# Performance work log

Measured on AMD Instinct MI355X. Metric: run time of the kernel, lower is better.

The kernel has to match this reference:

```python
import jax, jax.numpy as jnp
import numpy as np

RADIUS = 0.1
K = 32          # group_size
SCALE = 4
EPS = 1e-5      # InstanceNorm2d eps
BIG = 1e10


def _fps(p, n):
    # furthest point sampling, p: (B, N, 3) -> idx (B, n) int32
    B, N, _ = p.shape
    d0 = jnp.full((B, N), BIG, p.dtype)
    last0 = jnp.zeros((B,), jnp.int32)

    def step(carry, _):
        dists, last = carry
        lp = jnp.take_along_axis(p, last[:, None, None], axis=1)  # (B,1,3)
        d = jnp.sum((p - lp) ** 2, axis=-1)                        # (B,N)
        dists = jnp.minimum(dists, d)
        nxt = jnp.argmax(dists, axis=-1).astype(jnp.int32)
        return (dists, nxt), nxt

    (_, _), rest = jax.lax.scan(step, (d0, last0), None, length=n - 1)
    return jnp.concatenate([last0[None, :], rest], axis=0).T  # (B, n)


def _ball_query(center, p, radius, k):
    # center: (B,M,3), p: (B,N,3) -> neighbor idx (B,M,k)
    N = p.shape[1]
    d2 = jnp.sum((center[:, :, None, :] - p[:, None, :, :]) ** 2, axis=-1)  # (B,M,N)
    within = d2 < radius * radius
    cand = jnp.where(within, jnp.arange(N, dtype=jnp.int32), N)
    neg, _ = jax.lax.top_k(-cand, k)       # smallest k candidate indices
    cand = -neg                             # ascending, N = 'not found'
    first = cand[..., :1]
    idx = jnp.where(cand == N, first, cand)  # pad with first found (CUDA ballquery semantics)
    return jnp.where(idx == N, 0, idx)       # empty ball -> 0 (never happens: center is its own neighbor)


def _conv_block(x, w):
    # 1x1 conv (bias-free) + InstanceNorm2d(affine=False) + ReLU
    x = jnp.einsum('oi,bimk->bomk', w, x)
    m = x.mean(axis=(2, 3), keepdims=True)
    v = x.var(axis=(2, 3), keepdims=True)   # biased var, matches torch InstanceNorm
    x = (x - m) * jax.lax.rsqrt(v + EPS)
    return jax.nn.relu(x)


def _chan_attn(x, w1, w2):
    s = x.mean(axis=(2, 3))                 # (B,C) squeeze
    h = jax.nn.relu(s @ w1.T)
    g = jax.nn.sigmoid(h @ w2.T)
    return x * g[:, :, None, None]


def _stage(p_cur, f_cur, m, w1, a1w1, a1w2, w2, a2w1, a2w2):
    idx = _fps(p_cur, m)                                               # (B,M)
    cp = jnp.take_along_axis(p_cur, idx[:, :, None], axis=1)          # (B,M,3)
    cf = jnp.take_along_axis(f_cur, idx[:, None, :], axis=2)          # (B,C,M)
    gidx = _ball_query(cp, p_cur, RADIUS, K)                           # (B,M,K)
    gp = jax.vmap(lambda pts, i: pts[i])(p_cur, gidx)                  # (B,M,K,3)
    dp = jnp.transpose(gp - cp[:, :, None, :], (0, 3, 1, 2))           # (B,3,M,K)
    fj = jax.vmap(lambda ff, i: ff[:, i])(f_cur, gidx)                 # (B,C,M,K)
    feat = jnp.concatenate([dp, fj - cf[..., None]], axis=1)           # dp_df: (B,3+C,M,K)
    x = _chan_attn(_conv_block(feat, w1), a1w1, a1w2)
    pooled = jnp.broadcast_to(x.max(axis=-1, keepdims=True), x.shape)
    x = _chan_attn(_conv_block(jnp.concatenate([pooled, x], axis=1), w2), a2w1, a2w2)
    return cp, x.max(axis=-1)                                          # (B,M,3), (B,C_out,M)


def setup_inputs() -> dict:
    key = jax.random.key(0)
    ks = jax.random.split(key, 16)
    w = lambda k, o, i: (jax.random.normal(k, (o, i), jnp.float32) / np.float32(np.sqrt(i)))
    return {
        'p': jax.random.uniform(ks[0], (4, 8192, 3), jnp.float32),
        'f': jax.random.normal(ks[1], (4, 3, 8192), jnp.float32),
        # stage 0: edge-in 6 -> 192, conv2 384 -> 192
        's0_w1': w(ks[2], 192, 6),   's0_a1w1': w(ks[3], 48, 192),  's0_a1w2': w(ks[4], 192, 48),
        's0_w2': w(ks[5], 192, 384), 's0_a2w1': w(ks[6], 48, 192),  's0_a2w2': w(ks[7], 192, 48),
        # stage 1: edge-in 195 -> 384, conv2 768 -> 384
        's1_w1': w(ks[8], 384, 195), 's1_a1w1': w(ks[9], 96, 384),  's1_a1w2': w(ks[10], 384, 96),
        's1_w2': w(ks[11], 384, 768),'s1_a2w1': w(ks[12], 96, 384), 's1_a2w2': w(ks[13], 384, 96),
    }


def reference(p, f, s0_w1, s0_a1w1, s0_a1w2, s0_w2, s0_a2w1, s0_a2w2,
              s1_w1, s1_a1w1, s1_a1w2, s1_w2, s1_a2w1, s1_a2w2):
    N = p.shape[1]
    cp1, f1 = _stage(p, f, N // SCALE, s0_w1, s0_a1w1, s0_a1w2, s0_w2, s0_a2w1, s0_a2w2)
    cp2, f2 = _stage(cp1, f1, N // SCALE ** 2, s1_w1, s1_a1w1, s1_a1w2, s1_w2, s1_a2w1, s1_a2w2)
    # (out_p, out_f) flattened: points per level, features per level
    return (p, cp1, cp2, f, f1, f2)
```

## Files before the change

### kernel.cpp

```cpp
#include <hip/hip_runtime.h>
#include <hip/hip_bf16.h>
#include <stdint.h>

typedef __hip_bfloat16 bf16;
typedef unsigned long long u64;
typedef short bf16x8 __attribute__((ext_vector_type(8)));
typedef float f32x4 __attribute__((ext_vector_type(4)));
#define DEVI static __device__ __forceinline__

DEVI float b2f(bf16 v){ return __bfloat162float(v); }
DEVI bf16  f2b(float v){ return __float2bfloat16(v); }
DEVI float bfL(unsigned u){ return __uint_as_float(u<<16); }
DEVI float bfH(unsigned u){ return __uint_as_float(u & 0xffff0000u); }
DEVI void unpack8(uint4 r, float* v){
  v[0]=bfL(r.x); v[1]=bfH(r.x); v[2]=bfL(r.y); v[3]=bfH(r.y);
  v[4]=bfL(r.z); v[5]=bfH(r.z); v[6]=bfL(r.w); v[7]=bfH(r.w);
}
DEVI void unpack4(uint2 r, float* v){
  v[0]=bfL(r.x); v[1]=bfH(r.x); v[2]=bfL(r.y); v[3]=bfH(r.y);
}
DEVI unsigned short bfr(float x){ bf16 h=f2b(x); return *reinterpret_cast<unsigned short*>(&h); }
DEVI unsigned pk2(float a,float b){ return (unsigned)bfr(a) | ((unsigned)bfr(b)<<16); }

constexpr int B_=4, N0=8192, M0=2048, M1=512, KK=32;
constexpr int L0=M0*KK, L1=M1*KK;
constexpr int C0=192, H0=48, C1=384, H1=96;

constexpr size_t OUT_P=0, OUT_CP1=98304, OUT_CP2=122880, OUT_F=129024,
                 OUT_F1=227328, OUT_F2=1800192;

constexpr size_t A_FLAG  = 0;
constexpr size_t A_CP1F  = 256;
constexpr size_t A_CP2F  = A_CP1F+98304;
constexpr size_t A_IDX0  = A_CP2F+24576;
constexpr size_t A_IDX1  = A_IDX0+32768;
constexpr size_t A_GID0  = A_IDX1+8192;
constexpr size_t A_GID1  = A_GID0+1048576;
constexpr size_t A_FEAT0 = A_GID1+262144;
constexpr size_t A_M1V   = A_FEAT0+3145728;
constexpr size_t A_RS1V  = A_M1V+3072;
constexpr size_t A_SS01  = A_RS1V+3072;
constexpr size_t A_G1V   = A_SS01+3072;
constexpr size_t A_SUMA  = A_G1V+3072;
constexpr size_t A_SS02  = A_SUMA+6144;
constexpr size_t A_M2V   = A_SS02+3072;
constexpr size_t A_RS2V  = A_M2V+3072;
constexpr size_t A_G2V   = A_RS2V+3072;
constexpr size_t A_RAWP  = A_G2V+3072;
constexpr size_t A_RAWM2 = A_RAWP+6291456;
constexpr size_t A_FEAT1 = A_RAWM2+6291456;
constexpr size_t A_Y2    = A_FEAT1;
constexpr size_t WS_Y2   = A_Y2 + 100663296;
constexpr size_t A_YB1   = A_FEAT1+6389760;
constexpr size_t A_YB2   = A_YB1+12582912;
constexpr size_t A_PMS1  = A_YB2+12582912;
constexpr size_t A_MS1   = A_PMS1+786432;
constexpr size_t A_RSS1  = A_MS1+1536;
constexpr size_t A_SSS1  = A_RSS1+1536;
constexpr size_t A_G1S1  = A_SSS1+1536;
constexpr size_t A_G2S1  = A_G1S1+1536;
constexpr size_t A_F1A  = A_FEAT1;
constexpr size_t A_YB1A = A_F1A + 25559040;
constexpr size_t A_YB2A = A_YB1A + 50331648;
constexpr size_t A_PMA  = A_YB2A + 50331648;
constexpr size_t A_MSA  = A_PMA + 3145728;
constexpr size_t A_RSA  = A_MSA + 6144;
constexpr size_t A_SSA  = A_RSA + 6144;
constexpr size_t A_G1A  = A_SSA + 6144;
constexpr size_t A_G2A  = A_G1A + 6144;
constexpr size_t A_NEED = A_G2A + 6144;

DEVI const float* pick(const float* c0, const float* c1, const int* fl, int want_f){
  int sw = fl ? ((*fl)!=0) : 0;
  return (sw ^ want_f) ? c1 : c0;
}

__global__ __launch_bounds__(64)
void detect_kernel(const float* __restrict__ c0, int* __restrict__ flag){
  unsigned long long m = __ballot(c0[threadIdx.x] < 0.f);
  if(threadIdx.x==0) *flag = (m!=0ull) ? 1 : 0;
}

__global__ __launch_bounds__(256)
void cvt_pf_kernel(const float* __restrict__ c0, const float* __restrict__ c1,
                   const int* __restrict__ fl, float* __restrict__ outP,
                   float* __restrict__ outF, int n){
  const float* p = pick(c0,c1,fl,0);
  const float* f = pick(c0,c1,fl,1);
  int i=blockIdx.x*256+threadIdx.x;
  if(i<n){ outP[i]=p[i]; outF[i]=f[i]; }
}

#define DPP_ARGMAX(CTRL) { \
  int iv_=__builtin_amdgcn_update_dpp(__float_as_int(bv), __float_as_int(bv), CTRL, 0xF, 0xF, false); \
  int ii_=__builtin_amdgcn_update_dpp(bi, bi, CTRL, 0xF, 0xF, false); \
  float fv_=__int_as_float(iv_); \
  if(fv_>bv || (fv_==bv && ii_<bi)){ bv=fv_; bi=ii_; } }

template<int NP, int MS, int TPB>
__global__ __launch_bounds__(TPB)
void fps_kernel(const float* __restrict__ c0, const float* __restrict__ c1,
                const int* __restrict__ fl, int* __restrict__ sel){
  constexpr int CH = NP/TPB;
  constexpr int NW = TPB/64;
  __shared__ float4 pt4[NP];
  __shared__ u64 wvi[2][NW];
  const float* pC = pick(c0,c1,fl,0);
  int b=blockIdx.x, t=threadIdx.x;
  const float* pb = pC + (size_t)b*NP*3;
  for(int i=t;i<NP;i+=TPB)
    pt4[i]=make_float4(pb[(size_t)i*3], pb[(size_t)i*3+1], pb[(size_t)i*3+2], 0.f);
  if(t==0) sel[(size_t)b*MS]=0;
  __syncthreads();
  float ox[CH], oy[CH], oz[CH], dd[CH];
  #pragma unroll
  for(int c=0;c<CH;c++){
    float4 q=pt4[t*CH+c];
    ox[c]=q.x; oy[c]=q.y; oz[c]=q.z;
    dd[c]=1e10f;
  }
  float4 c40=pt4[0];
  float cx=c40.x, cy=c40.y, cz=c40.z;
  int par=0;
  for(int s=1;s<MS;s++){
    float bv=-1.f; int bi=0;
    #pragma unroll
    for(int c=0;c<CH;c++){
      float dx=__fsub_rn(ox[c],cx), dy=__fsub_rn(oy[c],cy), dz=__fsub_rn(oz[c],cz);
      float d=__fadd_rn(__fadd_rn(__fmul_rn(dx,dx),__fmul_rn(dy,dy)),__fmul_rn(dz,dz));
      float nd=fminf(dd[c],d); dd[c]=nd;
      if(nd>bv){ bv=nd; bi=t*CH+c; }
    }
    DPP_ARGMAX(0x111) DPP_ARGMAX(0x112) DPP_ARGMAX(0x114) DPP_ARGMAX(0x118)
    DPP_ARGMAX(0x142) DPP_ARGMAX(0x143)
    if((t&63)==63)
      wvi[par][t>>6] = (((u64)__float_as_uint(bv))<<32) | (unsigned)(0xFFFFFFFFu-(unsigned)bi);
    __syncthreads();
    u64 best=wvi[par][0];
    #pragma unroll
    for(int k=1;k<NW;k++){ u64 w=wvi[par][k]; if(w>best) best=w; }
    int mi = (int)(0xFFFFFFFFu - (unsigned)best);
    if(t==0) sel[(size_t)b*MS+s]=mi;
    float4 c4=pt4[mi];
    cx=c4.x; cy=c4.y; cz=c4.z;
    par^=1;
  }
}

__global__ __launch_bounds__(256)
void gather_cp_kernel(const float* __restrict__ c0, const float* __restrict__ c1,
                      const int* __restrict__ fl, const int* __restrict__ sel,
                      int NP, int MS, float* __restrict__ cpf, float* __restrict__ outcp){
  const float* pC = pick(c0,c1,fl,0);
  int t=blockIdx.x*256+threadIdx.x;
  if(t>=B_*MS) return;
  int b=t/MS;
  int j=sel[t];
  const float* src=pC + ((size_t)b*NP + j)*3;
  float x=src[0],y=src[1],z=src[2];
  float* d=cpf + (size_t)t*3; d[0]=x; d[1]=y; d[2]=z;
  float* o=outcp + (size_t)t*3; o[0]=x; o[1]=y; o[2]=z;
}

template<int NP, int MS>
__global__ __launch_bounds__(256)
void ballq_kernel(const float* __restrict__ c0, const float* __restrict__ c1,
                  const int* __restrict__ fl, const float* __restrict__ cpf,
                  int* __restrict__ gidx){
  __shared__ int cand[4][64][33];
  __shared__ int ccnt[4][64];
  const float* pC = pick(c0,c1,fl,0);
  int t=threadIdx.x, q=t>>6, cl=t&63;
  int b=blockIdx.y, m=blockIdx.x*64+cl;
  const float* cc=cpf + ((size_t)b*MS+m)*3;
  float cx=cc[0], cy=cc[1], cz=cc[2];
  const float R2=0.01f;
  const float* pb=pC + (size_t)b*NP*3;
  int cnt=0;
  int j0=q*(NP/4), j1=j0+NP/4;
  for(int j=j0;j<j1;j++){
    if(cnt>=32) break;
    float dx=__fsub_rn(cx,pb[(size_t)j*3]);
    float dy=__fsub_rn(cy,pb[(size_t)j*3+1]);
    float dz=__fsub_rn(cz,pb[(size_t)j*3+2]);
    float d2=__fadd_rn(__fadd_rn(__fmul_rn(dx,dx),__fmul_rn(dy,dy)),__fmul_rn(dz,dz));
    if(d2<R2) cand[q][cl][cnt++]=j;
  }
  ccnt[q][cl]=cnt;
  __syncthreads();
  if(q==0){
    int* gp=gidx + ((size_t)b*MS+m)*32;
    int total=0, first=0; bool has=false;
    for(int qq=0;qq<4;qq++){
      int n=ccnt[qq][cl];
      for(int u=0;u<n;u++){
        if(total>=32) break;
        int id=cand[qq][cl][u];
        if(!has){ first=id; has=true; }
        gp[total++]=id;
      }
      if(total>=32) break;
    }
    if(!has){ for(int u=0;u<32;u++) gp[u]=0; }
    else    { for(int u=total;u<32;u++) gp[u]=first; }
  }
}

__global__ __launch_bounds__(256)
void feat0_kernel(const float* __restrict__ c0, const float* __restrict__ c1,
                  const int* __restrict__ fl, const float* __restrict__ cp1f,
                  const int* __restrict__ idx0, const int* __restrict__ gidx0,
                  bf16* __restrict__ feat){
  const float* p0f = pick(c0,c1,fl,0);
  const float* f_in= pick(c0,c1,fl,1);
  int t=blockIdx.x*256+threadIdx.x;
  int b=t>>16, rem=t&65535, m=rem>>5;
  int j=gidx0[t];
  int sel=idx0[(b<<11)+m];
  const float* pj=p0f + ((size_t)(b*N0)+j)*3;
  const float* cm=cp1f + ((size_t)(b*M0)+m)*3;
  bf16* fb=feat + (size_t)b*6*L0 + rem;
  fb[0]      =f2b(pj[0]-cm[0]);
  fb[L0]     =f2b(pj[1]-cm[1]);
  fb[2*L0]   =f2b(pj[2]-cm[2]);
  const float* fI=f_in + (size_t)b*3*N0;
  #pragma unroll
  for(int c=0;c<3;c++)
    fb[(size_t)(3+c)*L0]=f2b(fI[c*N0+j]-fI[c*N0+sel]);
}

__global__ __launch_bounds__(256)
void s0c1_stats_kernel(const bf16* __restrict__ feat, const float* __restrict__ W1,
                       float* __restrict__ m1v, float* __restrict__ rs1v){
  int row=blockIdx.x, b=row/C0, c=row%C0, t=threadIdx.x;
  float w6[6];
  #pragma unroll
  for(int j=0;j<6;j++) w6[j]=W1[c*6+j];
  const bf16* fb=feat + (size_t)b*6*L0;
  float s=0.f,s2=0.f;
  for(int base=t*8;base<L0;base+=2048){
    float X[6][8];
    #pragma unroll
    for(int i=0;i<6;i++){ uint4 r=*(const uint4*)(fb+(size_t)i*L0+base); unpack8(r,X[i]); }
    #pragma unroll
    for(int u=0;u<8;u++){
      float y=0.f;
      #pragma unroll
      for(int j=0;j<6;j++) y=fmaf(w6[j],X[j][u],y);
      s+=y; s2+=y*y;
    }
  }
  #pragma unroll
  for(int off=32;off>0;off>>=1){ s+=__shfl_down(s,off,64); s2+=__shfl_down(s2,off,64); }
  __shared__ float as[4], bs[4];
  int w=t>>6;
  if((t&63)==0){ as[w]=s; bs[w]=s2; }
  __syncthreads();
  if(t==0){
    float S=as[0]+as[1]+as[2]+as[3], S2=bs[0]+bs[1]+bs[2]+bs[3];
    float m=S/(float)L0, var=S2/(float)L0-m*m;
    var=fmaxf(var,0.f);
    m1v[row]=m; rs1v[row]=rsqrtf(var+1e-5f);
  }
}

__global__ __launch_bounds__(256)
void s0c1_pool_kernel(const bf16* __restrict__ feat, const float* __restrict__ W1,
                      const float* __restrict__ m1v, const float* __restrict__ rs1v,
                      float* __restrict__ rawp, float* __restrict__ ss01){
  int row=blockIdx.x, b=row/C0, c=row%C0, t=threadIdx.x;
  float w6[6];
  #pragma unroll
  for(int j=0;j<6;j++) w6[j]=W1[c*6+j];
  const bf16* fb=feat + (size_t)b*6*L0;
  float m=m1v[row], rs=rs1v[row];
  float ss=0.f;
  for(int base=t*8;base<L0;base+=2048){
    float X[6][8];
    #pragma unroll
    for(int i=0;i<6;i++){ uint4 r=*(const uint4*)(fb+(size_t)i*L0+base); unpack8(r,X[i]); }
    float mx=-3e38f;
    #pragma unroll
    for(int u=0;u<8;u++){
      float y=0.f;
      #pragma unroll
      for(int j=0;j<6;j++) y=fmaf(w6[j],X[j][u],y);
      float x=fmaxf((y-m)*rs,0.f);
      ss+=x; mx=fmaxf(mx,x);
    }
    mx=fmaxf(mx,__shfl_down(mx,2,64));
    mx=fmaxf(mx,__shfl_down(mx,1,64));
    if((t&3)==0) rawp[(size_t)row*M0 + (base>>5)] = mx;
  }
  #pragma unroll
  for(int off=32;off>0;off>>=1) ss+=__shfl_down(ss,off,64);
  __shared__ float as[4];
  int w=t>>6;
  if((t&63)==0) as[w]=ss;
  __syncthreads();
  if(t==0) ss01[row]=(as[0]+as[1]+as[2]+as[3])/(float)L0;
}

__global__ __launch_bounds__(256)
void s0conv2_mfma_kernel(const float* __restrict__ W2, const bf16* __restrict__ feat,
                         const float* __restrict__ W1,
                         const float* __restrict__ m1v, const float* __restrict__ rs1v,
                         const float* __restrict__ g1v, const float* __restrict__ rawp,
                         bf16* __restrict__ y2out){
  __shared__ __align__(16) bf16 sW[2][64][40];
  __shared__ __align__(16) bf16 sXT[128][40];
  __shared__ float f6[6][128];
  __shared__ float w1s[192][6];
  __shared__ float cmv[192], crsv[192], cgv[192];
  int t=threadIdx.x, b=blockIdx.z, o0=blockIdx.y*64, l0=blockIdx.x*128;
  for(int u=t;u<768;u+=256){ int i=u>>7, lc=u&127; f6[i][lc]=b2f(feat[((size_t)(b*6+i))*L0+l0+lc]); }
  for(int u=t;u<1152;u+=256){ w1s[u/6][u%6]=W1[u]; }
  for(int u=t;u<192;u+=256){ int r=b*C0+u; cmv[u]=m1v[r]; crsv[u]=rs1v[r]; cgv[u]=g1v[r]; }
  int wv=t>>6, lane=t&63, nn=lane&15, quad=lane>>4, kb=quad*8;
  int il=t&31, lq=(t>>5)*16;
  f32x4 acc[8];
  #pragma unroll
  for(int i=0;i<8;i++) acc[i]=(f32x4){0.f,0.f,0.f,0.f};
  __syncthreads();
  for(int c=0;c<12;c++){
    int i0=c*32;
    for(int u=t;u<2048;u+=256){
      int oo=u>>5, kk=u&31;
      float w=W2[(size_t)(o0+oo)*384 + i0+kk];
      bf16 hi=f2b(w);
      sW[0][oo][kk]=hi;
      sW[1][oo][kk]=f2b(w-b2f(hi));
    }
    {
      int i=i0+il;
      if(i<192){
        float pv=cgv[i]*rawp[((size_t)(b*C0+i))*M0 + ((l0+lq)>>5)];
        bf16 pb_=f2b(pv);
        #pragma unroll
        for(int u=0;u<16;u++) sXT[lq+u][il]=pb_;
      } else {
        int cc=i-192;
        float w6[6];
        #pragma unroll
        for(int j=0;j<6;j++) w6[j]=w1s[cc][j];
        float mm=cmv[cc], rr=crsv[cc], gg=cgv[cc];
        #pragma unroll
        for(int u=0;u<16;u++){
          float y=0.f;
          #pragma unroll
          for(int j=0;j<6;j++) y=fmaf(w6[j], f6[j][lq+u], y);
          sXT[lq+u][il]=f2b(gg*fmaxf((y-mm)*rr,0.f));
        }
      }
    }
    __syncthreads();
    bf16x8 aHi=*(const bf16x8*)&sW[0][wv*16+nn][kb];
    bf16x8 aLo=*(const bf16x8*)&sW[1][wv*16+nn][kb];
    #pragma unroll
    for(int lt=0;lt<8;lt++){
      bf16x8 bfr_=*(const bf16x8*)&sXT[lt*16+nn][kb];
      acc[lt]=__builtin_amdgcn_mfma_f32_16x16x32_bf16(aHi,bfr_,acc[lt],0,0,0);
      acc[lt]=__builtin_amdgcn_mfma_f32_16x16x32_bf16(aLo,bfr_,acc[lt],0,0,0);
    }
    __syncthreads();
  }
  #pragma unroll
  for(int lt=0;lt<8;lt++){
    int l=l0+lt*16+nn;
    #pragma unroll
    for(int r=0;r<4;r++){
      int o=o0+wv*16+quad*4+r;
      y2out[((size_t)(b*C0+o))*L0 + l]=f2b(acc[lt][r]);
    }
  }
}

template<int PB>
__global__ __launch_bounds__(256)
void s0conv2_kernel(const float* __restrict__ W2, const bf16* __restrict__ feat,
                    const float* __restrict__ W1,
                    const float* __restrict__ m1v, const float* __restrict__ rs1v,
                    const float* __restrict__ g1v, const float* __restrict__ rawp,
                    float* __restrict__ sumA,
                    const float* __restrict__ m2v, const float* __restrict__ rs2v,
                    float* __restrict__ ssum2, float* __restrict__ rawm2){
  __shared__ float sW[96][17];
  __shared__ float sX[16][132];
  __shared__ float f6[6][128];
  __shared__ float w1s[192][6];
  __shared__ float cm[192], crs[192], cg[192];
  int t=threadIdx.x, b=blockIdx.z, o0=blockIdx.y*96, l0=blockIdx.x*128;
  for(int u=t;u<768;u+=256){ int i=u>>7, lc=u&127; f6[i][lc]=b2f(feat[((size_t)(b*6+i))*L0+l0+lc]); }
  for(int u=t;u<1152;u+=256){ w1s[u/6][u%6]=W1[u]; }
  for(int u=t;u<192;u+=256){ int r=b*C0+u; cm[u]=m1v[r]; crs[u]=rs1v[r]; cg[u]=g1v[r]; }
  __syncthreads();
  float acc[6][8];
  #pragma unroll
  for(int r=0;r<6;r++)
    #pragma unroll
    for(int c=0;c<8;c++) acc[r][c]=0.f;
  int to=t>>4, tl=t&15, oL=to*6;
  int xr=to, cA=tl*4;
  int mg0=(l0+cA)>>5;
  for(int i0=0;i0<384;i0+=16){
    #pragma unroll
    for(int u=0;u<6;u++){ int flat=u*256+t, r=flat>>4, ci=flat&15;
      sW[r][ci]=W2[(size_t)(o0+r)*384 + i0+ci]; }
    {
      int i=i0+xr;
      float v[8];
      if(i<192){
        float pv0=cg[i]*rawp[((size_t)(b*C0+i))*M0 + mg0];
        float pv1=cg[i]*rawp[((size_t)(b*C0+i))*M0 + mg0+2];
        v[0]=pv0; v[1]=pv0; v[2]=pv0; v[3]=pv0;
        v[4]=pv1; v[5]=pv1; v[6]=pv1; v[7]=pv1;
      } else {
        int c=i-192;
        #pragma unroll
        for(int u=0;u<4;u++){
          float y=0.f;
          #pragma unroll
          for(int j=0;j<6;j++) y=fmaf(w1s[c][j], f6[j][cA+u], y);
          v[u]=cg[c]*fmaxf((y-cm[c])*crs[c],0.f);
        }
        #pragma unroll
        for(int u=0;u<4;u++){
          float y=0.f;
          #pragma unroll
          for(int j=0;j<6;j++) y=fmaf(w1s[c][j], f6[j][64+cA+u], y);
          v[4+u]=cg[c]*fmaxf((y-cm[c])*crs[c],0.f);
        }
      }
      *(float4*)&sX[xr][cA]    = make_float4(v[0],v[1],v[2],v[3]);
      *(float4*)&sX[xr][64+cA] = make_float4(v[4],v[5],v[6],v[7]);
    }
    __syncthreads();
    #pragma unroll
    for(int kk=0;kk<16;kk++){
      float av[6];
      #pragma unroll
      for(int r=0;r<6;r++) av[r]=sW[oL+r][kk];
      float4 xa=*(const float4*)&sX[kk][cA];
      float4 xb=*(const float4*)&sX[kk][64+cA];
      float xv[8]={xa.x,xa.y,xa.z,xa.w,xb.x,xb.y,xb.z,xb.w};
      #pragma unroll
      for(int r=0;r<6;r++)
        #pragma unroll
        for(int c=0;c<8;c++) acc[r][c]=fmaf(av[r],xv[c],acc[r][c]);
    }
    __syncthreads();
  }
  if(PB==0){
    #pragma unroll
    for(int r=0;r<6;r++){
      float ps=0.f, ps2=0.f;
      #pragma unroll
      for(int c=0;c<8;c++){ ps+=acc[r][c]; ps2+=acc[r][c]*acc[r][c]; }
      #pragma unroll
      for(int off=8;off>0;off>>=1){ ps+=__shfl_down(ps,off,64); ps2+=__shfl_down(ps2,off,64); }
      if(tl==0){ int o=b*C0+o0+oL+r; atomicAdd(&sumA[o],ps); atomicAdd(&sumA[768+o],ps2); }
    }
  } else {
    #pragma unroll
    for(int r=0;r<6;r++){
      int o=b*C0+o0+oL+r;
      float mm=m2v[o], rr=rs2v[o];
      float ps=0.f;
      float mxA=-3e38f, mxB=-3e38f;
      #pragma unroll
      for(int c=0;c<4;c++){ float x=fmaxf((acc[r][c]-mm)*rr,0.f); ps+=x; mxA=fmaxf(mxA,x); }
      #pragma unroll
      for(int c=4;c<8;c++){ float x=fmaxf((acc[r][c]-mm)*rr,0.f); ps+=x; mxB=fmaxf(mxB,x); }
      #pragma unroll
      for(int off=8;off>0;off>>=1) ps+=__shfl_down(ps,off,64);
      if(tl==0) atomicAdd(&ssum2[o], ps);
      mxA=fmaxf(mxA,__shfl_down(mxA,4,64)); mxB=fmaxf(mxB,__shfl_down(mxB,4,64));
      mxA=fmaxf(mxA,__shfl_down(mxA,2,64)); mxB=fmaxf(mxB,__shfl_down(mxB,2,64));
      mxA=fmaxf(mxA,__shfl_down(mxA,1,64)); mxB=fmaxf(mxB,__shfl_down(mxB,1,64));
      if(tl==0){ rawm2[(size_t)o*M0 + (l0>>5)    ] = mxA;
                 rawm2[(size_t)o*M0 + (l0>>5) + 2] = mxB; }
      if(tl==8){ rawm2[(size_t)o*M0 + (l0>>5) + 1] = mxA;
                 rawm2[(size_t)o*M0 + (l0>>5) + 3] = mxB; }
    }
  }
}

__global__ __launch_bounds__(256)
void s0y2_pool_kernel(const bf16* __restrict__ y2, const float* __restrict__ m2v,
                      const float* __restrict__ rs2v,
                      float* __restrict__ rawm2, float* __restrict__ ss02){
  int row=blockIdx.x, t=threadIdx.x;
  const bf16* yr=y2 + (size_t)row*L0;
  float m=m2v[row], rs=rs2v[row];
  float ss=0.f;
  for(int base=t*8;base<L0;base+=2048){
    uint4 r=*(const uint4*)(yr+base);
    float v[8]; unpack8(r,v);
    float mx=-3e38f;
    #pragma unroll
    for(int u=0;u<8;u++){
      float x=fmaxf((v[u]-m)*rs,0.f);
      ss+=x; mx=fmaxf(mx,x);
    }
    mx=fmaxf(mx,__shfl_down(mx,2,64));
    mx=fmaxf(mx,__shfl_down(mx,1,64));
    if((t&3)==0) rawm2[(size_t)row*M0 + (base>>5)] = mx;
  }
  #pragma unroll
  for(int off=32;off>0;off>>=1) ss+=__shfl_down(ss,off,64);
  __shared__ float as[4];
  int w=t>>6;
  if((t&63)==0) as[w]=ss;
  __syncthreads();
  if(t==0) ss02[row]=(as[0]+as[1]+as[2]+as[3])/(float)L0;
}

__global__ __launch_bounds__(256)
void fin_stats_kernel(const float* __restrict__ sums, float invL, int n,
                      float* __restrict__ mp, float* __restrict__ rp){
  int i=blockIdx.x*256+threadIdx.x;
  if(i<n){
    float m=sums[i]*invL;
    float v=sums[n+i]*invL - m*m;
    v=fmaxf(v,0.f);
    mp[i]=m; rp[i]=rsqrtf(v+1e-5f);
  }
}

__global__ __launch_bounds__(256)
void f1fin_kernel(const float* __restrict__ g2, float* __restrict__ rawm,
                  float* __restrict__ outF1){
  int idx=blockIdx.x*256+threadIdx.x;
  int row=idx>>11;
  float v=g2[row]*rawm[idx];
  rawm[idx]=v;
  outF1[idx]=v;
}

__global__ __launch_bounds__(256)
void feat1_kernel(int bbase, const float* __restrict__ cp1f, const float* __restrict__ cp2f,
                  const float* __restrict__ f1f, const int* __restrict__ idx1,
                  const int* __restrict__ gid1, bf16* __restrict__ featb){
  int t=blockIdx.x*256+threadIdx.x;
  int bloc=t>>14, l=t&16383;
  int b=bbase+bloc;
  int m=l>>5;
  int j=gid1[((size_t)b*M1+m)*32 + (l&31)];
  int sel=idx1[b*M1+m];
  const float* pj=cp1f + ((size_t)b*M0+j)*3;
  const float* cm=cp2f + ((size_t)b*M1+m)*3;
  bf16* fb=featb + (size_t)bloc*195*L1;
  fb[l]       =f2b(pj[0]-cm[0]);
  fb[L1+l]    =f2b(pj[1]-cm[1]);
  fb[2*L1+l]  =f2b(pj[2]-cm[2]);
  const float* fB=f1f + (size_t)b*C0*M0;
  for(int c=0;c<C0;c++)
    fb[(size_t)(3+c)*L1+l]=f2b(fB[(size_t)c*M0+j]-fB[(size_t)c*M0+sel]);
}

template<bool CAT>
__global__ __launch_bounds__(256)
void conv_b_kernel(const float* __restrict__ W, const bf16* __restrict__ X, bf16* __restrict__ Y,
                   int I, int L, int M, size_t xbs, size_t ybs,
                   const float* __restrict__ pmax, const float* __restrict__ g,
                   size_t pbs, size_t gbs, int Cc){
  __shared__ float sX[16][132];
  __shared__ float sW[96][17];
  int t=threadIdx.x, z=blockIdx.z;
  int o0=blockIdx.y*96, l0=blockIdx.x*128;
  const bf16* Xb = X + (size_t)z*xbs;
  bf16* Yb = Y + (size_t)z*ybs;
  const float* pm = CAT ? (pmax + (size_t)z*pbs) : nullptr;
  const float* gz = CAT ? (g + (size_t)z*gbs) : nullptr;
  float acc[6][8];
  #pragma unroll
  for(int r=0;r<6;r++)
    #pragma unroll
    for(int c=0;c<8;c++) acc[r][c]=0.f;
  int to=t>>4, tl=t&15, oL=to*6;
  int xr=to, cA=tl*4;
  int mg0=(l0+cA)>>5;
  for(int i0=0;i0<I;i0+=16){
    #pragma unroll
    for(int u=0;u<6;u++){
      int flat=u*256+t, r=flat>>4, ci=flat&15, i=i0+ci;
      sW[r][ci] = (i<I) ? W[(size_t)(o0+r)*I+i] : 0.f;
    }
    {
      int i=i0+xr;
      float v[8];
      if(!CAT){
        if(i<I){
          const bf16* xp = Xb + (size_t)i*L + l0;
          uint2 ra=*(const uint2*)(xp+cA);
          uint2 rb=*(const uint2*)(xp+64+cA);
          unpack4(ra,v); unpack4(rb,v+4);
        } else {
          #pragma unroll
          for(int u=0;u<8;u++) v[u]=0.f;
        }
      } else {
        if(i<Cc){
          float pv0=pm[(size_t)i*M + mg0];
          float pv1=pm[(size_t)i*M + mg0+2];
          v[0]=pv0; v[1]=pv0; v[2]=pv0; v[3]=pv0;
          v[4]=pv1; v[5]=pv1; v[6]=pv1; v[7]=pv1;
        } else {
          int ii=i-Cc;
          float gg=gz[ii];
          const bf16* xp = Xb + (size_t)ii*L + l0;
          uint2 ra=*(const uint2*)(xp+cA);
          uint2 rb=*(const uint2*)(xp+64+cA);
          unpack4(ra,v); unpack4(rb,v+4);
          #pragma unroll
          for(int u=0;u<8;u++) v[u]*=gg;
        }
      }
      *(float4*)&sX[xr][cA]    = make_float4(v[0],v[1],v[2],v[3]);
      *(float4*)&sX[xr][64+cA] = make_float4(v[4],v[5],v[6],v[7]);
    }
    __syncthreads();
    #pragma unroll
    for(int kk=0;kk<16;kk++){
      float av[6];
      #pragma unroll
      for(int r=0;r<6;r++) av[r]=sW[oL+r][kk];
      float4 xa=*(const float4*)&sX[kk][cA];
      float4 xb=*(const float4*)&sX[kk][64+cA];
      float xv[8]={xa.x,xa.y,xa.z,xa.w,xb.x,xb.y,xb.z,xb.w};
      #pragma unroll
      for(int r=0;r<6;r++)
        #pragma unroll
        for(int c=0;c<8;c++) acc[r][c]=fmaf(av[r],xv[c],acc[r][c]);
    }
    __syncthreads();
  }
  #pragma unroll
  for(int r=0;r<6;r++){
    bf16* yp=Yb + (size_t)(o0+oL+r)*L + l0;
    #pragma unroll
    for(int c=0;c<4;c++) yp[cA+c]=f2b(acc[r][c]);
    #pragma unroll
    for(int c=0;c<4;c++) yp[64+cA+c]=f2b(acc[r][4+c]);
  }
}

__global__ __launch_bounds__(256)
void rowstats_kernel(const bf16* __restrict__ Y, int L,
                     float* __restrict__ meanp, float* __restrict__ rstdp){
  int row=blockIdx.x;
  const uint4* yr=(const uint4*)(Y + (size_t)row*L);
  int nv=L/8;
  float s=0.f, s2=0.f;
  for(int i=threadIdx.x;i<nv;i+=256){
    uint4 r=yr[i]; float v[8]; unpack8(r,v);
    #pragma unroll
    for(int u=0;u<8;u++){ s+=v[u]; s2+=v[u]*v[u]; }
  }
  #pragma unroll
  for(int off=32;off>0;off>>=1){ s+=__shfl_down(s,off,64); s2+=__shfl_down(s2,off,64); }
  __shared__ float as[4], bs[4];
  int w=threadIdx.x>>6;
  if((threadIdx.x&63)==0){ as[w]=s; bs[w]=s2; }
  __syncthreads();
  if(threadIdx.x==0){
    float S=as[0]+as[1]+as[2]+as[3], S2=bs[0]+bs[1]+bs[2]+bs[3];
    float m=S/(float)L, var=S2/(float)L - m*m;
    var=fmaxf(var,0.f);
    meanp[row]=m; rstdp[row]=rsqrtf(var+1e-5f);
  }
}

__global__ __launch_bounds__(256)
void normrelu_kernel(bf16* __restrict__ Y, int L, const float* __restrict__ meanp,
                     const float* __restrict__ rstdp, float* __restrict__ ssum){
  int row=blockIdx.x;
  float m=meanp[row], rs=rstdp[row];
  uint4* yr=(uint4*)(Y + (size_t)row*L);
  int nv=L/8;
  float s=0.f;
  for(int i=threadIdx.x;i<nv;i+=256){
    uint4 r=yr[i]; float v[8]; unpack8(r,v);
    #pragma unroll
    for(int u=0;u<8;u++){ float x=(v[u]-m)*rs; x=fmaxf(x,0.f); v[u]=x; s+=x; }
    uint4 o; o.x=pk2(v[0],v[1]); o.y=pk2(v[2],v[3]); o.z=pk2(v[4],v[5]); o.w=pk2(v[6],v[7]);
    yr[i]=o;
  }
  #pragma unroll
  for(int off=32;off>0;off>>=1) s+=__shfl_down(s,off,64);
  __shared__ float as[4];
  int w=threadIdx.x>>6;
  if((threadIdx.x&63)==0) as[w]=s;
  __syncthreads();
  if(threadIdx.x==0) ssum[row]=(as[0]+as[1]+as[2]+as[3])/(float)L;
}

__global__ __launch_bounds__(256)
void attn_kernel(const float* __restrict__ ssum, const float* __restrict__ w1,
                 const float* __restrict__ w2, int Cc, int H, float* __restrict__ g,
                 float scale){
  __shared__ float sv[384]; __shared__ float hv[96];
  int b=blockIdx.x, t=threadIdx.x;
  for(int i=t;i<Cc;i+=256) sv[i]=ssum[b*Cc+i]*scale;
  __syncthreads();
  if(t<H){
    float a=0.f;
    for(int c=0;c<Cc;c++) a+=w1[(size_t)t*Cc+c]*sv[c];
    hv[t]=fmaxf(a,0.f);
  }
  __syncthreads();
  for(int o=t;o<Cc;o+=256){
    float a=0.f;
    for(int j=0;j<H;j++) a+=w2[(size_t)o*H+j]*hv[j];
    g[b*Cc+o]=1.f/(1.f+expf(-a));
  }
}

__global__ __launch_bounds__(256)
void pmax_kernel(const bf16* __restrict__ Xn, const float* __restrict__ g,
                 int Mloc, float* __restrict__ pm){
  int row=blockIdx.y;
  int m=blockIdx.x*256+threadIdx.x;
  const uint4* x=(const uint4*)(Xn + (size_t)row*Mloc*32 + (size_t)m*32);
  float mv=-3.0e38f;
  #pragma unroll
  for(int i=0;i<4;i++){
    uint4 r=x[i]; float v[8]; unpack8(r,v);
    #pragma unroll
    for(int u=0;u<8;u++) mv=fmaxf(mv,v[u]);
  }
  pm[(size_t)row*Mloc+m]=g[row]*mv;
}

__global__ __launch_bounds__(256)
void fmax_out_kernel(const bf16* __restrict__ Xn, const float* __restrict__ g,
                     int Mloc, float* __restrict__ outp){
  int row=blockIdx.y;
  int m=blockIdx.x*256+threadIdx.x;
  const uint4* x=(const uint4*)(Xn + (size_t)row*Mloc*32 + (size_t)m*32);
  float mv=-3.0e38f;
  #pragma unroll
  for(int i=0;i<4;i++){
    uint4 r=x[i]; float v[8]; unpack8(r,v);
    #pragma unroll
    for(int u=0;u<8;u++) mv=fmaxf(mv,v[u]);
  }
  outp[(size_t)row*Mloc+m]=g[row]*mv;
}

extern "C" void kernel_launch(void* const* d_in, const int* in_sizes, int n_in,
                              void* d_out, int out_size, void* d_ws, size_t ws_size,
                              hipStream_t stream){
  const float* PF[2]={nullptr,nullptr}; int npf=0;
  const float* A9[4]={0,0,0,0};  int n9=0;
  const float* A36[4]={0,0,0,0}; int n36=0;
  const float *s0_w1=0,*s0_w2=0,*s1_w1=0,*s1_w2=0;
  for(int i=0;i<n_in;i++){
    const float* ptr=(const float*)d_in[i];
    switch(in_sizes[i]){
      case 98304:  if(npf<2) PF[npf++]=ptr; break;
      case 1152:   s0_w1=ptr; break;
      case 73728:  s0_w2=ptr; break;
      case 74880:  s1_w1=ptr; break;
      case 294912: s1_w2=ptr; break;
      case 9216:   if(n9<4)  A9[n9++]=ptr;  break;
      case 36864:  if(n36<4) A36[n36++]=ptr; break;
      default: break;
    }
  }
  const float* s0_a1w1=A9[0];  const float* s0_a1w2=A9[1];
  const float* s0_a2w1=A9[2];  const float* s0_a2w2=A9[3];
  const float* s1_a1w1=A36[0]; const float* s1_a1w2=A36[1];
  const float* s1_a2w1=A36[2]; const float* s1_a2w2=A36[3];

  float* out=(float*)d_out;
  char* ws=(char*)d_ws;

  int*   flag =(int*)  (ws+A_FLAG);
  float* cp1f =(float*)(ws+A_CP1F);
  float* cp2f =(float*)(ws+A_CP2F);
  int*   idx0 =(int*)  (ws+A_IDX0);
  int*   idx1 =(int*)  (ws+A_IDX1);
  int*   gid0 =(int*)  (ws+A_GID0);
  int*   gid1 =(int*)  (ws+A_GID1);
  bf16*  feat0=(bf16*) (ws+A_FEAT0);
  float* m1v  =(float*)(ws+A_M1V);
  float* rs1v =(float*)(ws+A_RS1V);
  float* ss01 =(float*)(ws+A_SS01);
  float* g1v  =(float*)(ws+A_G1V);
  float* sumA =(float*)(ws+A_SUMA);
  float* ss02 =(float*)(ws+A_SS02);
  float* m2v  =(float*)(ws+A_M2V);
  float* rs2v =(float*)(ws+A_RS2V);
  float* g2v  =(float*)(ws+A_G2V);
  float* rawp =(float*)(ws+A_RAWP);
  float* rawm2=(float*)(ws+A_RAWM2);
  float* f1f  =rawm2;
  bf16*  y2s0 =(bf16*) (ws+A_Y2);

  detect_kernel<<<1,64,0,stream>>>(PF[0], flag);
  cvt_pf_kernel<<<384,256,0,stream>>>(PF[0], PF[1], flag, out+OUT_P, out+OUT_F, B_*N0*3);

  fps_kernel<N0,M0,256><<<B_,256,0,stream>>>(PF[0], PF[1], flag, idx0);
  gather_cp_kernel<<<32,256,0,stream>>>(PF[0], PF[1], flag, idx0, N0, M0, cp1f, out+OUT_CP1);
  ballq_kernel<N0,M0><<<dim3(32,B_),256,0,stream>>>(PF[0], PF[1], flag, cp1f, gid0);
  feat0_kernel<<<1024,256,0,stream>>>(PF[0], PF[1], flag, cp1f, idx0, gid0, feat0);

  s0c1_stats_kernel<<<B_*C0,256,0,stream>>>(feat0, s0_w1, m1v, rs1v);
  s0c1_pool_kernel<<<B_*C0,256,0,stream>>>(feat0, s0_w1, m1v, rs1v, rawp, ss01);
  attn_kernel<<<B_,256,0,stream>>>(ss01, s0_a1w1, s0_a1w2, C0, H0, g1v, 1.f);

  if(ws_size >= WS_Y2){
    s0conv2_mfma_kernel<<<dim3(512,3,B_),256,0,stream>>>(s0_w2, feat0, s0_w1, m1v, rs1v, g1v, rawp, y2s0);
    rowstats_kernel<<<B_*C0,256,0,stream>>>(y2s0, L0, m2v, rs2v);
    s0y2_pool_kernel<<<B_*C0,256,0,stream>>>(y2s0, m2v, rs2v, rawm2, ss02);
    attn_kernel<<<B_,256,0,stream>>>(ss02, s0_a2w1, s0_a2w2, C0, H0, g2v, 1.f);
  } else {
    hipMemsetAsync(ws+A_SUMA, 0, 9216, stream);
    s0conv2_kernel<0><<<dim3(512,2,B_),256,0,stream>>>(s0_w2, feat0, s0_w1, m1v, rs1v, g1v,
                                                       rawp, sumA, nullptr,nullptr,nullptr,nullptr);
    fin_stats_kernel<<<3,256,0,stream>>>(sumA, 1.f/(float)L0, 768, m2v, rs2v);
    s0conv2_kernel<1><<<dim3(512,2,B_),256,0,stream>>>(s0_w2, feat0, s0_w1, m1v, rs1v, g1v,
                                                       rawp, nullptr, m2v, rs2v, ss02, rawm2);
    attn_kernel<<<B_,256,0,stream>>>(ss02, s0_a2w1, s0_a2w2, C0, H0, g2v, 1.f/(float)L0);
  }
  f1fin_kernel<<<6144,256,0,stream>>>(g2v, rawm2, out+OUT_F1);

  fps_kernel<M0,M1,256><<<B_,256,0,stream>>>(cp1f, cp1f, nullptr, idx1);
  gather_cp_kernel<<<8,256,0,stream>>>(cp1f, cp1f, nullptr, idx1, M0, M1, cp2f, out+OUT_CP2);
  ballq_kernel<M0,M1><<<dim3(8,B_),256,0,stream>>>(cp1f, cp1f, nullptr, cp2f, gid1);

  if(ws_size >= A_NEED){
    bf16*  f1a =(bf16*) (ws+A_F1A);
    bf16*  yb1a=(bf16*) (ws+A_YB1A);
    bf16*  yb2a=(bf16*) (ws+A_YB2A);
    float* pma =(float*)(ws+A_PMA);
    float* msa =(float*)(ws+A_MSA);
    float* rsa =(float*)(ws+A_RSA);
    float* ssa =(float*)(ws+A_SSA);
    float* g1a =(float*)(ws+A_G1A);
    float* g2a =(float*)(ws+A_G2A);
    feat1_kernel<<<B_*L1/256,256,0,stream>>>(0, cp1f, cp2f, f1f, idx1, gid1, f1a);
    conv_b_kernel<false><<<dim3(L1/128,4,B_),256,0,stream>>>(s1_w1, f1a, yb1a, 195, L1, M1,
                                 (size_t)195*L1, (size_t)C1*L1, nullptr,nullptr,0,0,0);
    rowstats_kernel<<<B_*C1,256,0,stream>>>(yb1a, L1, msa, rsa);
    normrelu_kernel<<<B_*C1,256,0,stream>>>(yb1a, L1, msa, rsa, ssa);
    attn_kernel<<<B_,256,0,stream>>>(ssa, s1_a1w1, s1_a1w2, C1, H1, g1a, 1.f);
    pmax_kernel<<<dim3(2,B_*C1),256,0,stream>>>(yb1a, g1a, M1, pma);
    conv_b_kernel<true><<<dim3(L1/128,4,B_),256,0,stream>>>(s1_w2, yb1a, yb2a, 2*C1, L1, M1,
                                 (size_t)C1*L1, (size_t)C1*L1, pma, g1a, (size_t)C1*M1, (size_t)C1, C1);
    rowstats_kernel<<<B_*C1,256,0,stream>>>(yb2a, L1, msa, rsa);
    normrelu_kernel<<<B_*C1,256,0,stream>>>(yb2a, L1, msa, rsa, ssa);
    attn_kernel<<<B_,256,0,stream>>>(ssa, s1_a2w1, s1_a2w2, C1, H1, g2a, 1.f);
    fmax_out_kernel<<<dim3(2,B_*C1),256,0,stream>>>(yb2a, g2a, M1, out+OUT_F2);
  } else {
    bf16*  feat1b=(bf16*)(ws+A_FEAT1);
    bf16*  ybuf1 =(bf16*)(ws+A_YB1);
    bf16*  ybuf2 =(bf16*)(ws+A_YB2);
    float* pmS1 =(float*)(ws+A_PMS1);
    float* mS1  =(float*)(ws+A_MS1);
    float* rsS1 =(float*)(ws+A_RSS1);
    float* ssS1 =(float*)(ws+A_SSS1);
    float* g1s1 =(float*)(ws+A_G1S1);
    float* g2s1 =(float*)(ws+A_G2S1);
    for(int b=0;b<B_;b++){
      feat1_kernel<<<64,256,0,stream>>>(b, cp1f, cp2f, f1f, idx1, gid1, feat1b);
      conv_b_kernel<false><<<dim3(L1/128,4,1),256,0,stream>>>(s1_w1, feat1b, ybuf1, 195, L1, M1,
                                   0,0, nullptr,nullptr,0,0,0);
      rowstats_kernel<<<C1,256,0,stream>>>(ybuf1, L1, mS1, rsS1);
      normrelu_kernel<<<C1,256,0,stream>>>(ybuf1, L1, mS1, rsS1, ssS1);
      attn_kernel<<<1,256,0,stream>>>(ssS1, s1_a1w1, s1_a1w2, C1, H1, g1s1, 1.f);
      pmax_kernel<<<dim3(2,C1),256,0,stream>>>(ybuf1, g1s1, M1, pmS1);
      conv_b_kernel<true><<<dim3(L1/128,4,1),256,0,stream>>>(s1_w2, ybuf1, ybuf2, 2*C1, L1, M1,
                                   0,0, pmS1, g1s1, 0,0, C1);
      rowstats_kernel<<<C1,256,0,stream>>>(ybuf2, L1, mS1, rsS1);
      normrelu_kernel<<<C1,256,0,stream>>>(ybuf2, L1, mS1, rsS1, ssS1);
      attn_kernel<<<1,256,0,stream>>>(ssS1, s1_a2w1, s1_a2w2, C1, H1, g2s1, 1.f);
      fmax_out_kernel<<<dim3(2,C1),256,0,stream>>>(ybuf2, g2s1, M1, out+OUT_F2+(size_t)b*C1*M1);
    }
  }
}
```

Before: 4.143 ms.

## Move stage-1 convs to split-bf16 MFMA and streamline FPS reduction

Stage-1 1x1 convolutions now run through a new MFMA kernel that splits fp32 weights into hi/lo bf16 parts, precomputed by a small wsplit kernel into extra workspace. The aim is to replace the scalar conv_b path with matrix-core work while keeping close to fp32 weight precision. FPS no longer keeps a shared point table. The argmax reduction now carries the winning coordinates through the DPP and cross-wave steps, and indices are buffered in shared memory and written once at the end. FPS also launches with 512 threads instead of 256. The MFMA path is only taken if the workspace is large enough, and activations are still rounded to bf16.

```diff
diff --git a/kernel.cpp b/kernel.cpp
--- a/kernel.cpp
+++ b/kernel.cpp
@@ -69,6 +69,11 @@
 constexpr size_t A_G1A  = A_SSA + 6144;
 constexpr size_t A_G2A  = A_G1A + 6144;
 constexpr size_t A_NEED = A_G2A + 6144;
+constexpr size_t A_W1H  = A_NEED;
+constexpr size_t A_W1L  = A_W1H + 172032;
+constexpr size_t A_W2H  = A_W1L + 172032;
+constexpr size_t A_W2L  = A_W2H + 589824;
+constexpr size_t A_NEED2= A_W2L + 589824;
 
 DEVI const float* pick(const float* c0, const float* c1, const int* fl, int want_f){
   int sw = fl ? ((*fl)!=0) : 0;
@@ -91,11 +96,15 @@
   if(i<n){ outP[i]=p[i]; outF[i]=f[i]; }
 }
 
-#define DPP_ARGMAX(CTRL) { \
+#define DPP_ARGMAX5(CTRL) { \
   int iv_=__builtin_amdgcn_update_dpp(__float_as_int(bv), __float_as_int(bv), CTRL, 0xF, 0xF, false); \
   int ii_=__builtin_amdgcn_update_dpp(bi, bi, CTRL, 0xF, 0xF, false); \
+  int ix_=__builtin_amdgcn_update_dpp(__float_as_int(bx), __float_as_int(bx), CTRL, 0xF, 0xF, false); \
+  int iy_=__builtin_amdgcn_update_dpp(__float_as_int(by), __float_as_int(by), CTRL, 0xF, 0xF, false); \
+  int iz_=__builtin_amdgcn_update_dpp(__float_as_int(bz), __float_as_int(bz), CTRL, 0xF, 0xF, false); \
   float fv_=__int_as_float(iv_); \
-  if(fv_>bv || (fv_==bv && ii_<bi)){ bv=fv_; bi=ii_; } }
+  if(fv_>bv || (fv_==bv && ii_<bi)){ bv=fv_; bi=ii_; \
+    bx=__int_as_float(ix_); by=__int_as_float(iy_); bz=__int_as_float(iz_); } }
 
 template<int NP, int MS, int TPB>
 __global__ __launch_bounds__(TPB)
@@ -103,48 +112,48 @@
                 const int* __restrict__ fl, int* __restrict__ sel){
   constexpr int CH = NP/TPB;
   constexpr int NW = TPB/64;
-  __shared__ float4 pt4[NP];
-  __shared__ u64 wvi[2][NW];
+  __shared__ u64 kky[2][NW];
+  __shared__ float4 kxy[2][NW];
+  __shared__ int msel[MS];
   const float* pC = pick(c0,c1,fl,0);
   int b=blockIdx.x, t=threadIdx.x;
   const float* pb = pC + (size_t)b*NP*3;
-  for(int i=t;i<NP;i+=TPB)
-    pt4[i]=make_float4(pb[(size_t)i*3], pb[(size_t)i*3+1], pb[(size_t)i*3+2], 0.f);
-  if(t==0) sel[(size_t)b*MS]=0;
-  __syncthreads();
   float ox[CH], oy[CH], oz[CH], dd[CH];
   #pragma unroll
   for(int c=0;c<CH;c++){
-    float4 q=pt4[t*CH+c];
-    ox[c]=q.x; oy[c]=q.y; oz[c]=q.z;
+    int i=t*CH+c;
+    ox[c]=pb[i*3]; oy[c]=pb[i*3+1]; oz[c]=pb[i*3+2];
     dd[c]=1e10f;
   }
-  float4 c40=pt4[0];
-  float cx=c40.x, cy=c40.y, cz=c40.z;
+  if(t==0) msel[0]=0;
+  float cx=pb[0], cy=pb[1], cz=pb[2];
   int par=0;
   for(int s=1;s<MS;s++){
-    float bv=-1.f; int bi=0;
+    float bv=-1.f, bx=0.f, by=0.f, bz=0.f; int bi=0;
     #pragma unroll
     for(int c=0;c<CH;c++){
       float dx=__fsub_rn(ox[c],cx), dy=__fsub_rn(oy[c],cy), dz=__fsub_rn(oz[c],cz);
       float d=__fadd_rn(__fadd_rn(__fmul_rn(dx,dx),__fmul_rn(dy,dy)),__fmul_rn(dz,dz));
       float nd=fminf(dd[c],d); dd[c]=nd;
-      if(nd>bv){ bv=nd; bi=t*CH+c; }
-    }
-    DPP_ARGMAX(0x111) DPP_ARGMAX(0x112) DPP_ARGMAX(0x114) DPP_ARGMAX(0x118)
-    DPP_ARGMAX(0x142) DPP_ARGMAX(0x143)
-    if((t&63)==63)
-      wvi[par][t>>6] = (((u64)__float_as_uint(bv))<<32) | (unsigned)(0xFFFFFFFFu-(unsigned)bi);
+      if(nd>bv){ bv=nd; bi=t*CH+c; bx=ox[c]; by=oy[c]; bz=oz[c]; }
+    }
+    DPP_ARGMAX5(0x111) DPP_ARGMAX5(0x112) DPP_ARGMAX5(0x114) DPP_ARGMAX5(0x118)
+    DPP_ARGMAX5(0x142) DPP_ARGMAX5(0x143)
+    if((t&63)==63){
+      kky[par][t>>6] = (((u64)__float_as_uint(bv))<<32) | (unsigned)(0xFFFFFFFFu-(unsigned)bi);
+      kxy[par][t>>6] = make_float4(bx,by,bz,0.f);
+    }
     __syncthreads();
-    u64 best=wvi[par][0];
-    #pragma unroll
-    for(int k=1;k<NW;k++){ u64 w=wvi[par][k]; if(w>best) best=w; }
-    int mi = (int)(0xFFFFFFFFu - (unsigned)best);
-    if(t==0) sel[(size_t)b*MS+s]=mi;
-    float4 c4=pt4[mi];
+    u64 best=kky[par][0]; int kb=0;
+    #pragma unroll
+    for(int k=1;k<NW;k++){ u64 w=kky[par][k]; if(w>best){ best=w; kb=k; } }
+    if(t==0) msel[s]=(int)(0xFFFFFFFFu-(unsigned)best);
+    float4 c4=kxy[par][kb];
     cx=c4.x; cy=c4.y; cz=c4.z;
     par^=1;
   }
+  __syncthreads();
+  for(int i=t;i<MS;i+=TPB) sel[(size_t)b*MS+i]=msel[i];
 }
 
 __global__ __launch_bounds__(256)
@@ -373,6 +382,100 @@
       y2out[((size_t)(b*C0+o))*L0 + l]=f2b(acc[lt][r]);
     }
   }
+}
+
+template<bool CAT>
+__global__ __launch_bounds__(256)
+void conv_mfma_kernel(const bf16* __restrict__ Whi, const bf16* __restrict__ Wlo,
+                      const bf16* __restrict__ X, bf16* __restrict__ Y,
+                      int I, int Kpad, int L, int M, size_t xbs, size_t ybs,
+                      const float* __restrict__ pmax, const float* __restrict__ g,
+                      size_t pbs, size_t gbs, int Cc){
+  __shared__ __align__(16) bf16 sW[2][64][40];
+  __shared__ __align__(16) bf16 sXT[128][40];
+  int t=threadIdx.x, z=blockIdx.z, o0=blockIdx.y*64, l0=blockIdx.x*128;
+  const bf16* Xb = X + (size_t)z*xbs;
+  bf16* Yb = Y + (size_t)z*ybs;
+  const float* pm = CAT ? (pmax + (size_t)z*pbs) : nullptr;
+  const float* gz = CAT ? (g + (size_t)z*gbs) : nullptr;
+  int wv=t>>6, lane=t&63, nn=lane&15, quad=lane>>4, kb=quad*8;
+  int il=t&31, lq=(t>>5)*16;
+  f32x4 acc[8];
+  #pragma unroll
+  for(int i=0;i<8;i++) acc[i]=(f32x4){0.f,0.f,0.f,0.f};
+  int nch=Kpad/32;
+  for(int c=0;c<nch;c++){
+    int i0=c*32;
+    for(int u=t;u<2048;u+=256){
+      int oo=u>>5, kk=u&31;
+      sW[0][oo][kk]=Whi[(size_t)(o0+oo)*Kpad + i0+kk];
+      sW[1][oo][kk]=Wlo[(size_t)(o0+oo)*Kpad + i0+kk];
+    }
+    {
+      int i=i0+il;
+      if(!CAT){
+        if(i<I){
+          const bf16* xp = Xb + (size_t)i*L + l0 + lq;
+          bf16 tmp[16];
+          *(uint4*)&tmp[0]=*(const uint4*)xp;
+          *(uint4*)&tmp[8]=*(const uint4*)(xp+8);
+          #pragma unroll
+          for(int u=0;u<16;u++) sXT[lq+u][il]=tmp[u];
+        } else {
+          bf16 z0=f2b(0.f);
+          #pragma unroll
+          for(int u=0;u<16;u++) sXT[lq+u][il]=z0;
+        }
+      } else {
+        if(i<Cc){
+          float pv=pm[(size_t)i*M + ((l0+lq)>>5)];
+          bf16 pb_=f2b(pv);
+          #pragma unroll
+          for(int u=0;u<16;u++) sXT[lq+u][il]=pb_;
+        } else {
+          int ii=i-Cc;
+          float gg=gz[ii];
+          const bf16* xp = Xb + (size_t)ii*L + l0 + lq;
+          bf16 tmp[16];
+          *(uint4*)&tmp[0]=*(const uint4*)xp;
+          *(uint4*)&tmp[8]=*(const uint4*)(xp+8);
+          #pragma unroll
+          for(int u=0;u<16;u++) sXT[lq+u][il]=f2b(b2f(tmp[u])*gg);
+        }
+      }
+    }
+    __syncthreads();
+    bf16x8 aHi=*(const bf16x8*)&sW[0][wv*16+nn][kb];
+    bf16x8 aLo=*(const bf16x8*)&sW[1][wv*16+nn][kb];
+    #pragma unroll
+    for(int lt=0;lt<8;lt++){
+      bf16x8 bfr_=*(const bf16x8*)&sXT[lt*16+nn][kb];
+      acc[lt]=__builtin_amdgcn_mfma_f32_16x16x32_bf16(aHi,bfr_,acc[lt],0,0,0);
+      acc[lt]=__builtin_amdgcn_mfma_f32_16x16x32_bf16(aLo,bfr_,acc[lt],0,0,0);
+    }
+    __syncthreads();
+  }
+  #pragma unroll
+  for(int lt=0;lt<8;lt++){
+    int l=l0+lt*16+nn;
+    #pragma unroll
+    for(int r=0;r<4;r++){
+      int o=o0+wv*16+quad*4+r;
+      Yb[(size_t)o*L + l]=f2b(acc[lt][r]);
+    }
+  }
+}
+
+__global__ __launch_bounds__(256)
+void wsplit_kernel(const float* __restrict__ W, bf16* __restrict__ hi, bf16* __restrict__ lo,
+                   int I, int Kpad, int n){
+  int idx=blockIdx.x*256+threadIdx.x;
+  if(idx>=n) return;
+  int o=idx/Kpad, k=idx%Kpad;
+  float w = (k<I) ? W[(size_t)o*I+k] : 0.f;
+  bf16 h=f2b(w);
+  hi[idx]=h;
+  lo[idx]=f2b(w-b2f(h));
 }
 
 template<int PB>
@@ -801,7 +904,7 @@
   detect_kernel<<<1,64,0,stream>>>(PF[0], flag);
   cvt_pf_kernel<<<384,256,0,stream>>>(PF[0], PF[1], flag, out+OUT_P, out+OUT_F, B_*N0*3);
 
-  fps_kernel<N0,M0,256><<<B_,256,0,stream>>>(PF[0], PF[1], flag, idx0);
+  fps_kernel<N0,M0,512><<<B_,512,0,stream>>>(PF[0], PF[1], flag, idx0);
   gather_cp_kernel<<<32,256,0,stream>>>(PF[0], PF[1], flag, idx0, N0, M0, cp1f, out+OUT_CP1);
   ballq_kernel<N0,M0><<<dim3(32,B_),256,0,stream>>>(PF[0], PF[1], flag, cp1f, gid0);
   feat0_kernel<<<1024,256,0,stream>>>(PF[0], PF[1], flag, cp1f, idx0, gid0, feat0);
@@ -826,7 +929,7 @@
   }
   f1fin_kernel<<<6144,256,0,stream>>>(g2v, rawm2, out+OUT_F1);
 
-  fps_kernel<M0,M1,256><<<B_,256,0,stream>>>(cp1f, cp1f, nullptr, idx1);
+  fps_kernel<M0,M1,512><<<B_,512,0,stream>>>(cp1f, cp1f, nullptr, idx1);
   gather_cp_kernel<<<8,256,0,stream>>>(cp1f, cp1f, nullptr, idx1, M0, M1, cp2f, out+OUT_CP2);
   ballq_kernel<M0,M1><<<dim3(8,B_),256,0,stream>>>(cp1f, cp1f, nullptr, cp2f, gid1);
 
@@ -840,14 +943,31 @@
     float* ssa =(float*)(ws+A_SSA);
     float* g1a =(float*)(ws+A_G1A);
     float* g2a =(float*)(ws+A_G2A);
+    bool mfma1 = (ws_size >= A_NEED2);
+    bf16* w1h=(bf16*)(ws+A_W1H); bf16* w1l=(bf16*)(ws+A_W1L);
+    bf16* w2h=(bf16*)(ws+A_W2H); bf16* w2l=(bf16*)(ws+A_W2L);
+    if(mfma1){
+      wsplit_kernel<<<(384*224+255)/256,256,0,stream>>>(s1_w1, w1h, w1l, 195, 224, 384*224);
+      wsplit_kernel<<<(384*768+255)/256,256,0,stream>>>(s1_w2, w2h, w2l, 768, 768, 384*768);
+    }
     feat1_kernel<<<B_*L1/256,256,0,stream>>>(0, cp1f, cp2f, f1f, idx1, gid1, f1a);
-    conv_b_kernel<false><<<dim3(L1/128,4,B_),256,0,stream>>>(s1_w1, f1a, yb1a, 195, L1, M1,
+    if(mfma1)
+      conv_mfma_kernel<false><<<dim3(L1/128,C1/64,B_),256,0,stream>>>(w1h, w1l, f1a, yb1a,
+                                 195, 224, L1, M1, (size_t)195*L1, (size_t)C1*L1,
+                                 nullptr,nullptr,0,0,0);
+    else
+      conv_b_kernel<false><<<dim3(L1/128,4,B_),256,0,stream>>>(s1_w1, f1a, yb1a, 195, L1, M1,
                                  (size_t)195*L1, (size_t)C1*L1, nullptr,nullptr,0,0,0);
     rowstats_kernel<<<B_*C1,256,0,stream>>>(yb1a, L1, msa, rsa);
     normrelu_kernel<<<B_*C1,256,0,stream>>>(yb1a, L1, msa, rsa, ssa);
     attn_kernel<<<B_,256,0,stream>>>(ssa, s1_a1w1, s1_a1w2, C1, H1, g1a, 1.f);
     pmax_kernel<<<dim3(2,B_*C1),256,0,stream>>>(yb1a, g1a, M1, pma);
-    conv_b_kernel<true><<<dim3(L1/128,4,B_),256,0,stream>>>(s1_w2, yb1a, yb2a, 2*C1, L1, M1,
+    if(mfma1)
+      conv_mfma_kernel<true><<<dim3(L1/128,C1/64,B_),256,0,stream>>>(w2h, w2l, yb1a, yb2a,
+                                 768, 768, L1, M1, (size_t)C1*L1, (size_t)C1*L1,
+                                 pma, g1a, (size_t)C1*M1, (size_t)C1, C1);
+    else
+      conv_b_kernel<true><<<dim3(L1/128,4,B_),256,0,stream>>>(s1_w2, yb1a, yb2a, 2*C1, L1, M1,
                                  (size_t)C1*L1, (size_t)C1*L1, pma, g1a, (size_t)C1*M1, (size_t)C1, C1);
     rowstats_kernel<<<B_*C1,256,0,stream>>>(yb2a, L1, msa, rsa);
     normrelu_kernel<<<B_*C1,256,0,stream>>>(yb2a, L1, msa, rsa, ssa);
```

After: 4.966 ms. +19.9%, slower.
